# Optimization experiments

Measured on AMD Instinct MI355X. Metric: run time of the kernel, lower is better.

The kernel has to match this reference:

```python
import jax, jax.numpy as jnp
import numpy as np

N_NODES = 150000
N_USERS = 100000
EMB = 64
N_EDGES = 4800000
N_LAYERS = 3


def setup_inputs() -> dict:
    key = jax.random.key(0)
    k1, k2, k3, k4 = jax.random.split(key, 4)
    emb_weight = jax.random.normal(k1, (N_NODES, EMB), dtype=jnp.float32)
    adj_row = jnp.sort(jax.random.randint(k2, (N_EDGES,), 0, N_NODES, dtype=jnp.int64))
    adj_col = jax.random.randint(k3, (N_EDGES,), 0, N_NODES, dtype=jnp.int64)
    adj_vals = jax.random.uniform(k4, (N_EDGES,), dtype=jnp.float32)
    return {
        "emb_weight": emb_weight,
        "adj_row": adj_row,
        "adj_col": adj_col,
        "adj_vals": adj_vals,
        "n_users": N_USERS,
        "n_nodes": N_NODES,
        "n_layers": N_LAYERS,
    }


def _spmm(row, col, vals, x, n_nodes):
    # COO SpMM: out[r] += vals[e] * x[col[e]]  for each edge e with row[e]==r
    gathered = x[col] * vals[:, None]            # [nnz, emb]
    return jax.ops.segment_sum(gathered, row, num_segments=n_nodes)


def reference(emb_weight, adj_row, adj_col, adj_vals, n_users, n_nodes, n_layers):
    all_emb = emb_weight
    embs_sum = all_emb                           # running sum instead of stack+mean
    for _ in range(n_layers):
        all_emb = _spmm(adj_row, adj_col, adj_vals, all_emb, n_nodes)
        embs_sum = embs_sum + all_emb
    final_emb = embs_sum / jnp.asarray(n_layers + 1, dtype=emb_weight.dtype)
    users = final_emb[:n_users]
    items = final_emb[n_users:]
    return (users, items)
```

## Files before the change

kernel.cpp:

```cpp
#include <hip/hip_runtime.h>

#define EMB 64

__device__ __forceinline__ float bl(unsigned int u) { return __uint_as_float(u << 16); }
__device__ __forceinline__ float bh(unsigned int u) { return __uint_as_float(u & 0xffff0000u); }
__device__ __forceinline__ unsigned int pack2(float a, float b) {
    unsigned int ua = __float_as_uint(a); ua += 0x7fffu + ((ua >> 16) & 1u);
    unsigned int ub = __float_as_uint(b); ub += 0x7fffu + ((ub >> 16) & 1u);
    return (ua >> 16) | (ub & 0xffff0000u);
}

__global__ void __launch_bounds__(256) k_rowptr(const int* __restrict__ row,
                                                int* __restrict__ ptr, int E, int R) {
    int e = blockIdx.x * blockDim.x + threadIdx.x;
    if (e >= E) return;
    int r = row[e];
    int prev = (e == 0) ? -1 : row[e - 1];
    for (int q = prev + 1; q <= r; ++q) ptr[q] = e;
    if (e == E - 1) {
        for (int q = r + 1; q <= R; ++q) ptr[q] = E;
    }
}

__global__ void __launch_bounds__(256) k_prep(const float* __restrict__ emb,
                                              uint4* __restrict__ Xb, int n8) {
    int i = blockIdx.x * blockDim.x + threadIdx.x;
    if (i >= n8) return;
    const float4* p = reinterpret_cast<const float4*>(emb) + (size_t)i * 2;
    float4 a = p[0], b = p[1];
    uint4 x;
    x.x = pack2(a.x, a.y); x.y = pack2(a.z, a.w);
    x.z = pack2(b.x, b.y); x.w = pack2(b.z, b.w);
    Xb[i] = x;
}

__device__ __forceinline__ void loadcv(const int* __restrict__ col,
                                       const float* __restrict__ vals,
                                       int idx, int lim, int& c, float& v) {
    int i = idx < lim ? idx : lim - 1;
    c = col[i];
    v = (idx < lim) ? vals[i] : 0.f;
}

__global__ void __launch_bounds__(256) k_spmm(const int* __restrict__ ptr,
                                              const int* __restrict__ col,
                                              const float* __restrict__ vals,
                                              const uint4* __restrict__ Xb,
                                              uint4* __restrict__ Yb, int R) {
    int tid = blockIdx.x * blockDim.x + threadIdx.x;
    int g   = tid >> 3;
    int gl  = tid & 7;
    if (g >= R) return;

    int s = ptr[g];
    int e = ptr[g + 1];

    if (s >= e) {
        Yb[(size_t)g * 8 + gl] = make_uint4(0u, 0u, 0u, 0u);
        return;
    }

    float acc0 = 0.f, acc1 = 0.f, acc2 = 0.f, acc3 = 0.f;
    float acc4 = 0.f, acc5 = 0.f, acc6 = 0.f, acc7 = 0.f;

    int   c0, c1;
    float v0, v1;
    loadcv(col, vals, s + gl,     e, c0, v0);
    loadcv(col, vals, s + 8 + gl, e, c1, v1);

    for (int base = s; base < e; base += 16) {
        int   cj[16];
        float vj[16];
        #pragma unroll
        for (int j = 0; j < 8; ++j) {
            cj[j]     = __shfl(c0, j, 8);
            vj[j]     = __shfl(v0, j, 8);
            cj[8 + j] = __shfl(c1, j, 8);
            vj[8 + j] = __shfl(v1, j, 8);
        }
        uint4 xv[16];
        #pragma unroll
        for (int j = 0; j < 16; ++j)
            xv[j] = Xb[(size_t)cj[j] * 8 + gl];
        int nbase = base + 16;
        if (nbase < e) {
            loadcv(col, vals, nbase + gl,     e, c0, v0);
            loadcv(col, vals, nbase + 8 + gl, e, c1, v1);
        }
        #pragma unroll
        for (int j = 0; j < 16; ++j) {
            acc0 = fmaf(vj[j], bl(xv[j].x), acc0);
            acc1 = fmaf(vj[j], bh(xv[j].x), acc1);
            acc2 = fmaf(vj[j], bl(xv[j].y), acc2);
            acc3 = fmaf(vj[j], bh(xv[j].y), acc3);
            acc4 = fmaf(vj[j], bl(xv[j].z), acc4);
            acc5 = fmaf(vj[j], bh(xv[j].z), acc5);
            acc6 = fmaf(vj[j], bl(xv[j].w), acc6);
            acc7 = fmaf(vj[j], bh(xv[j].w), acc7);
        }
    }

    uint4 y;
    y.x = pack2(acc0, acc1); y.y = pack2(acc2, acc3);
    y.z = pack2(acc4, acc5); y.w = pack2(acc6, acc7);
    Yb[(size_t)g * 8 + gl] = y;
}

__global__ void __launch_bounds__(256) k_final(const float* __restrict__ emb,
                                               const uint4* __restrict__ X1,
                                               const uint4* __restrict__ X2,
                                               const uint4* __restrict__ X3,
                                               float* __restrict__ out, int n8) {
    int i = blockIdx.x * blockDim.x + threadIdx.x;
    if (i >= n8) return;
    const float4* p = reinterpret_cast<const float4*>(emb) + (size_t)i * 2;
    float4 a = p[0], b = p[1];
    uint4 x1 = X1[i], x2 = X2[i], x3 = X3[i];
    float4 o0, o1;
    o0.x = 0.25f * (a.x + bl(x1.x) + bl(x2.x) + bl(x3.x));
    o0.y = 0.25f * (a.y + bh(x1.x) + bh(x2.x) + bh(x3.x));
    o0.z = 0.25f * (a.z + bl(x1.y) + bl(x2.y) + bl(x3.y));
    o0.w = 0.25f * (a.w + bh(x1.y) + bh(x2.y) + bh(x3.y));
    o1.x = 0.25f * (b.x + bl(x1.z) + bl(x2.z) + bl(x3.z));
    o1.y = 0.25f * (b.y + bh(x1.z) + bh(x2.z) + bh(x3.z));
    o1.z = 0.25f * (b.z + bl(x1.w) + bl(x2.w) + bl(x3.w));
    o1.w = 0.25f * (b.w + bh(x1.w) + bh(x2.w) + bh(x3.w));
    float4* q = reinterpret_cast<float4*>(out) + (size_t)i * 2;
    q[0] = o0; q[1] = o1;
}

extern "C" void kernel_launch(void* const* d_in, const int* in_sizes, int n_in,
                              void* d_out, int out_size, void* d_ws, size_t ws_size,
                              hipStream_t stream) {
    const float* emb  = (const float*)d_in[0];
    const int*   row  = (const int*)d_in[1];
    const int*   col  = (const int*)d_in[2];
    const float* vals = (const float*)d_in[3];

    int nemb = in_sizes[0];
    int E    = in_sizes[1];
    int R    = nemb / EMB;

    uint4* X0  = (uint4*)d_ws;
    uint4* X1  = X0 + nemb / 8;
    uint4* X2  = X1 + nemb / 8;
    uint4* X3  = X2 + nemb / 8;
    int*   ptr = (int*)(X3 + nemb / 8);

    dim3 blk(256);
    int gridE    = (E + 255) / 256;
    int gridElem = (nemb / 8 + 255) / 256;
    int gridRows = (R * 8 + 255) / 256;

    k_rowptr<<<gridE, blk, 0, stream>>>(row, ptr, E, R);
    k_prep<<<gridElem, blk, 0, stream>>>(emb, X0, nemb / 8);

    k_spmm<<<gridRows, blk, 0, stream>>>(ptr, col, vals, X0, X1, R);
    k_spmm<<<gridRows, blk, 0, stream>>>(ptr, col, vals, X1, X2, R);
    k_spmm<<<gridRows, blk, 0, stream>>>(ptr, col, vals, X2, X3, R);

    k_final<<<gridElem, blk, 0, stream>>>(emb, X1, X2, X3, (float*)d_out, nemb / 8);
}
```

Baseline: 280.7 us.

## Fuse final averaging into last SpMM layer and load edge indices directly

```diff
diff --git a/kernel.cpp b/kernel.cpp
--- a/kernel.cpp
+++ b/kernel.cpp
@@ -34,19 +34,16 @@
     Xb[i] = x;
 }
 
-__device__ __forceinline__ void loadcv(const int* __restrict__ col,
-                                       const float* __restrict__ vals,
-                                       int idx, int lim, int& c, float& v) {
-    int i = idx < lim ? idx : lim - 1;
-    c = col[i];
-    v = (idx < lim) ? vals[i] : 0.f;
-}
-
-__global__ void __launch_bounds__(256) k_spmm(const int* __restrict__ ptr,
-                                              const int* __restrict__ col,
-                                              const float* __restrict__ vals,
-                                              const uint4* __restrict__ Xb,
-                                              uint4* __restrict__ Yb, int R) {
+template <int FINAL>
+__global__ void __launch_bounds__(256, 3) k_spmm(const int* __restrict__ ptr,
+                                                 const int* __restrict__ col,
+                                                 const float* __restrict__ vals,
+                                                 const uint4* __restrict__ Xb,
+                                                 uint4* __restrict__ Yb,
+                                                 const float* __restrict__ emb,
+                                                 const uint4* __restrict__ Xa,
+                                                 const uint4* __restrict__ Xc,
+                                                 float* __restrict__ out, int R) {
     int tid = blockIdx.x * blockDim.x + threadIdx.x;
     int g   = tid >> 3;
     int gl  = tid & 7;
@@ -55,78 +52,61 @@
     int s = ptr[g];
     int e = ptr[g + 1];
 
-    if (s >= e) {
-        Yb[(size_t)g * 8 + gl] = make_uint4(0u, 0u, 0u, 0u);
-        return;
-    }
-
     float acc0 = 0.f, acc1 = 0.f, acc2 = 0.f, acc3 = 0.f;
     float acc4 = 0.f, acc5 = 0.f, acc6 = 0.f, acc7 = 0.f;
 
-    int   c0, c1;
-    float v0, v1;
-    loadcv(col, vals, s + gl,     e, c0, v0);
-    loadcv(col, vals, s + 8 + gl, e, c1, v1);
-
-    for (int base = s; base < e; base += 16) {
-        int   cj[16];
-        float vj[16];
-        #pragma unroll
-        for (int j = 0; j < 8; ++j) {
-            cj[j]     = __shfl(c0, j, 8);
-            vj[j]     = __shfl(v0, j, 8);
-            cj[8 + j] = __shfl(c1, j, 8);
-            vj[8 + j] = __shfl(v1, j, 8);
-        }
-        uint4 xv[16];
-        #pragma unroll
-        for (int j = 0; j < 16; ++j)
-            xv[j] = Xb[(size_t)cj[j] * 8 + gl];
-        int nbase = base + 16;
-        if (nbase < e) {
-            loadcv(col, vals, nbase + gl,     e, c0, v0);
-            loadcv(col, vals, nbase + 8 + gl, e, c1, v1);
-        }
-        #pragma unroll
-        for (int j = 0; j < 16; ++j) {
-            acc0 = fmaf(vj[j], bl(xv[j].x), acc0);
-            acc1 = fmaf(vj[j], bh(xv[j].x), acc1);
-            acc2 = fmaf(vj[j], bl(xv[j].y), acc2);
-            acc3 = fmaf(vj[j], bh(xv[j].y), acc3);
-            acc4 = fmaf(vj[j], bl(xv[j].z), acc4);
-            acc5 = fmaf(vj[j], bh(xv[j].z), acc5);
-            acc6 = fmaf(vj[j], bl(xv[j].w), acc6);
-            acc7 = fmaf(vj[j], bh(xv[j].w), acc7);
+    if (s < e) {
+        for (int base = s; base < e; base += 16) {
+            int   cv[16];
+            float vv[16];
+            #pragma unroll
+            for (int j = 0; j < 16; ++j) {
+                int idx = base + j;
+                int i2  = idx < e ? idx : e - 1;
+                cv[j] = col[i2];
+                vv[j] = vals[i2];
+            }
+            uint4 xv[16];
+            #pragma unroll
+            for (int j = 0; j < 16; ++j)
+                xv[j] = Xb[(size_t)((unsigned)cv[j] * 8u + (unsigned)gl)];
+            #pragma unroll
+            for (int j = 0; j < 16; ++j) {
+                float v = (base + j < e) ? vv[j] : 0.f;
+                acc0 = fmaf(v, bl(xv[j].x), acc0);
+                acc1 = fmaf(v, bh(xv[j].x), acc1);
+                acc2 = fmaf(v, bl(xv[j].y), acc2);
+                acc3 = fmaf(v, bh(xv[j].y), acc3);
+                acc4 = fmaf(v, bl(xv[j].z), acc4);
+                acc5 = fmaf(v, bh(xv[j].z), acc5);
+                acc6 = fmaf(v, bl(xv[j].w), acc6);
+                acc7 = fmaf(v, bh(xv[j].w), acc7);
+            }
         }
     }
 
-    uint4 y;
-    y.x = pack2(acc0, acc1); y.y = pack2(acc2, acc3);
-    y.z = pack2(acc4, acc5); y.w = pack2(acc6, acc7);
-    Yb[(size_t)g * 8 + gl] = y;
-}
-
-__global__ void __launch_bounds__(256) k_final(const float* __restrict__ emb,
-                                               const uint4* __restrict__ X1,
-                                               const uint4* __restrict__ X2,
-                                               const uint4* __restrict__ X3,
-                                               float* __restrict__ out, int n8) {
-    int i = blockIdx.x * blockDim.x + threadIdx.x;
-    if (i >= n8) return;
-    const float4* p = reinterpret_cast<const float4*>(emb) + (size_t)i * 2;
-    float4 a = p[0], b = p[1];
-    uint4 x1 = X1[i], x2 = X2[i], x3 = X3[i];
-    float4 o0, o1;
-    o0.x = 0.25f * (a.x + bl(x1.x) + bl(x2.x) + bl(x3.x));
-    o0.y = 0.25f * (a.y + bh(x1.x) + bh(x2.x) + bh(x3.x));
-    o0.z = 0.25f * (a.z + bl(x1.y) + bl(x2.y) + bl(x3.y));
-    o0.w = 0.25f * (a.w + bh(x1.y) + bh(x2.y) + bh(x3.y));
-    o1.x = 0.25f * (b.x + bl(x1.z) + bl(x2.z) + bl(x3.z));
-    o1.y = 0.25f * (b.y + bh(x1.z) + bh(x2.z) + bh(x3.z));
-    o1.z = 0.25f * (b.z + bl(x1.w) + bl(x2.w) + bl(x3.w));
-    o1.w = 0.25f * (b.w + bh(x1.w) + bh(x2.w) + bh(x3.w));
-    float4* q = reinterpret_cast<float4*>(out) + (size_t)i * 2;
-    q[0] = o0; q[1] = o1;
+    if (FINAL) {
+        const float4* er = reinterpret_cast<const float4*>(emb + (size_t)g * EMB + gl * 8);
+        float4 a = er[0], b = er[1];
+        uint4 x1 = Xa[(size_t)g * 8 + gl];
+        uint4 x2 = Xc[(size_t)g * 8 + gl];
+        float4 o0, o1;
+        o0.x = 0.25f * (a.x + bl(x1.x) + bl(x2.x) + acc0);
+        o0.y = 0.25f * (a.y + bh(x1.x) + bh(x2.x) + acc1);
+        o0.z = 0.25f * (a.z + bl(x1.y) + bl(x2.y) + acc2);
+        o0.w = 0.25f * (a.w + bh(x1.y) + bh(x2.y) + acc3);
+        o1.x = 0.25f * (b.x + bl(x1.z) + bl(x2.z) + acc4);
+        o1.y = 0.25f * (b.y + bh(x1.z) + bh(x2.z) + acc5);
+        o1.z = 0.25f * (b.z + bl(x1.w) + bl(x2.w) + acc6);
+        o1.w = 0.25f * (b.w + bh(x1.w) + bh(x2.w) + acc7);
+        float4* q = reinterpret_cast<float4*>(out + (size_t)g * EMB + gl * 8);
+        q[0] = o0; q[1] = o1;
+    } else {
+        uint4 y;
+        y.x = pack2(acc0, acc1); y.y = pack2(acc2, acc3);
+        y.z = pack2(acc4, acc5); y.w = pack2(acc6, acc7);
+        Yb[(size_t)g * 8 + gl] = y;
+    }
 }
 
 extern "C" void kernel_launch(void* const* d_in, const int* in_sizes, int n_in,
@@ -144,8 +124,7 @@
     uint4* X0  = (uint4*)d_ws;
     uint4* X1  = X0 + nemb / 8;
     uint4* X2  = X1 + nemb / 8;
-    uint4* X3  = X2 + nemb / 8;
-    int*   ptr = (int*)(X3 + nemb / 8);
+    int*   ptr = (int*)(X2 + nemb / 8);
 
     dim3 blk(256);
     int gridE    = (E + 255) / 256;
@@ -155,9 +134,11 @@
     k_rowptr<<<gridE, blk, 0, stream>>>(row, ptr, E, R);
     k_prep<<<gridElem, blk, 0, stream>>>(emb, X0, nemb / 8);
 
-    k_spmm<<<gridRows, blk, 0, stream>>>(ptr, col, vals, X0, X1, R);
-    k_spmm<<<gridRows, blk, 0, stream>>>(ptr, col, vals, X1, X2, R);
-    k_spmm<<<gridRows, blk, 0, stream>>>(ptr, col, vals, X2, X3, R);
-
-    k_final<<<gridElem, blk, 0, stream>>>(emb, X1, X2, X3, (float*)d_out, nemb / 8);
+    float* outp = (float*)d_out;
+    k_spmm<0><<<gridRows, blk, 0, stream>>>(ptr, col, vals, X0, X1,
+                                            emb, X0, X0, outp, R);
+    k_spmm<0><<<gridRows, blk, 0, stream>>>(ptr, col, vals, X1, X2,
+                                            emb, X0, X0, outp, R);
+    k_spmm<1><<<gridRows, blk, 0, stream>>>(ptr, col, vals, X2, X1,
+                                            emb, X1, X2, outp, R);
 }
```

Result: slower. 293.9 us (+4.7%).
